# Performance work log

Measured on AMD Instinct MI355X. Metric: run time of the kernel, lower is better.

The kernel has to match this reference:

```python
import jax, jax.numpy as jnp
import numpy as np

C = 1.0          # curvature parameter (constraint <x,x>_L = -1/C)
EPS = 1e-7
N_NODES = 50000
D = 128
N_EDGES = 800000


def _l_inner(u, v):
    # Lorentz (Minkowski) inner product: -u0*v0 + <u_s, v_s>
    return -u[..., 0] * v[..., 0] + jnp.sum(u[..., 1:] * v[..., 1:], axis=-1)


def _proj(x, c=C):
    # recompute time coordinate so x lies on the hyperboloid
    sp = x[:, 1:]
    x0 = jnp.sqrt(1.0 / c + jnp.sum(sp * sp, axis=-1, keepdims=True))
    return jnp.concatenate([x0, sp], axis=-1)


def _logmap0(x, c=C):
    sqc = jnp.sqrt(c)
    x0, sp = x[:, :1], x[:, 1:]
    y = jnp.clip(sqc * x0, 1.0 + EPS, None)
    d = jnp.arccosh(y) / sqc                                   # geodesic distance to origin
    sn = jnp.clip(jnp.linalg.norm(sp, axis=-1, keepdims=True), EPS, None)
    return jnp.concatenate([jnp.zeros_like(x0), d * sp / sn], axis=-1)


def _expmap0(u, c=C):
    sqc = jnp.sqrt(c)
    sp = u[:, 1:]
    un = jnp.clip(jnp.linalg.norm(sp, axis=-1, keepdims=True), EPS, None)
    th = sqc * un
    x0 = jnp.cosh(th) / sqc
    return jnp.concatenate([x0, jnp.sinh(th) * sp / th], axis=-1)


def setup_inputs() -> dict:
    key = jax.random.key(0)
    k1, k2, k3 = jax.random.split(key, 3)
    x_raw = jax.random.normal(k1, (N_NODES, D), dtype=jnp.float32) * 0.5
    x = _proj(x_raw)  # valid points on the Lorentz manifold
    # xavier-uniform-like scale for (127,127) weight
    lim = float(np.sqrt(6.0 / (2 * (D - 1))))
    weight = jax.random.uniform(k2, (D - 1, D - 1), dtype=jnp.float32, minval=-lim, maxval=lim)
    bias = jnp.zeros((D - 1,), dtype=jnp.float32)
    edge_index = jax.random.randint(k3, (2, N_EDGES), 0, N_NODES, dtype=jnp.int64)
    return {"x": x, "weight": weight, "bias": bias, "edge_index": edge_index}


def reference(x, weight, bias, edge_index):
    c = C
    # ---- HyperbolicLinear (lorentz): log0 -> spatial matmul + bias -> exp0 -> proj
    v = _logmap0(x, c)                         # [N, D], time comp = 0
    out_space = v[:, 1:] @ weight.T + bias     # [N, D-1]
    out = jnp.concatenate([v[:, :1], out_space], axis=-1)
    h = _proj(_expmap0(out, c), c)             # [N, D] on manifold
    # ---- HyperbolicDistAtt: gather -> lorentz distance -> exp(-d)
    row, col = edge_index[0], edge_index[1]
    xi = h[row]                                # [E, D]
    xj = h[col]                                # [E, D]
    inner = _l_inner(xi, xj)                   # [E]
    dist = jnp.arccosh(jnp.clip(-c * inner, 1.0 + EPS, None)) / jnp.sqrt(c)
    att = jnp.exp(-dist)                       # [E]
    # ---- Lorentz centroid: weighted sum then Minkowski-norm normalization
    num = jax.ops.segment_sum(att[:, None] * xj, row, num_segments=h.shape[0])  # [N, D]
    denom = jnp.sqrt(c) * jnp.sqrt(jnp.clip(-_l_inner(num, num), EPS, None))    # [N]
    return num / denom[:, None]
```

## Files before the change

### kernel.cpp

```cpp
#include <hip/hip_runtime.h>
#include <math.h>

#define EPS 1e-7f
#define CAP 64
#define REC_INTS   34
#define REC_USH    68
#define LIST_OFF    4

typedef __attribute__((ext_vector_type(8))) short short8;
typedef __attribute__((ext_vector_type(4))) float floatx4;
typedef _Float16 half2v __attribute__((ext_vector_type(2)));

__device__ inline short f2bf(float f) {
    union { float f; unsigned u; } v; v.f = f;
    unsigned r = v.u + 0x7FFF + ((v.u >> 16) & 1);
    return (short)(r >> 16);
}
__device__ inline ushort f2h(float f) {
    union { _Float16 h; ushort u; } v; v.h = (_Float16)f; return v.u;
}
__device__ inline half2v u2h2(unsigned u) {
    union { unsigned x; half2v h; } v; v.x = u; return v.h;
}
__device__ inline float dot2acc(unsigned a, unsigned b, float c) {
#if __has_builtin(__builtin_amdgcn_fdot2)
    return __builtin_amdgcn_fdot2(u2h2(a), u2h2(b), c, false);
#else
    half2v ha = u2h2(a), hb = u2h2(b);
    return c + (float)ha[0] * (float)hb[0] + (float)ha[1] * (float)hb[1];
#endif
}

__device__ inline float fast_sqrt(float x) { return __builtin_amdgcn_sqrtf(x); }
__device__ inline float fast_rcp(float x)  { return __builtin_amdgcn_rcpf(x); }
__device__ inline float fast_rsq(float x)  { return __builtin_amdgcn_rsqf(x); }

__global__ __launch_bounds__(256) void prep_w(
    const float* __restrict__ weight, short* __restrict__ wfg,
    int* __restrict__ rec, int N)
{
    int idx = blockIdx.x * 256 + threadIdx.x;
    if (idx < 128 * 128) {
        int j = idx >> 7, k = idx & 127;
        float w = (j < 127 && k >= 1) ? weight[j * 127 + (k - 1)] : 0.0f;
        int tt = j >> 4, cc = j & 15, ss = k >> 5, qq = (k >> 3) & 3, ee = k & 7;
        wfg[(((tt * 4 + ss) * 64) + qq * 16 + cc) * 8 + ee] = f2bf(w);
    }
    if (rec) {
        for (int r = idx; r < N; r += gridDim.x * 256) rec[(size_t)r * REC_INTS] = 0;
    }
}

__global__ __launch_bounds__(256) void transform16(
    const float* __restrict__ x, const short* __restrict__ wfg,
    const float* __restrict__ bias, ushort* __restrict__ h16, int N)
{
    __shared__ __align__(16) short Vf[4 * 4 * 64 * 8];

    const int t = threadIdx.x;
    const int lane = t & 63;
    const int wv = t >> 6;
    const int c = lane & 15;
    const int q = lane >> 4;

    float bvals[8];
    #pragma unroll
    for (int tt = 0; tt < 8; ++tt) {
        int j = tt * 16 + c;
        bvals[tt] = (j < 127) ? bias[j] : 0.0f;
    }

    const short8* wfp = (const short8*)wfg;
    const short8* vfp = (const short8*)Vf + wv * 256;
    short8* vw = (short8*)Vf;

    const int nchunks = (N + 63) >> 6;
    for (int chunk = blockIdx.x; chunk < nchunks; chunk += gridDim.x) {
        const int base = chunk * 64;

        {
            int nl = t >> 2;
            int qt = t & 3;
            int n = base + nl;
            const float4* xr = (const float4*)(x + (size_t)n * 128 + qt * 32);
            float4 xv[8];
            if (n < N) {
                #pragma unroll
                for (int g = 0; g < 8; ++g) xv[g] = xr[g];
            } else {
                #pragma unroll
                for (int g = 0; g < 8; ++g) xv[g] = make_float4(0, 0, 0, 0);
            }
            float ss = 0.0f;
            #pragma unroll
            for (int g = 0; g < 8; ++g)
                ss += xv[g].x * xv[g].x + xv[g].y * xv[g].y +
                      xv[g].z * xv[g].z + xv[g].w * xv[g].w;
            float x0 = xv[0].x;
            if (qt == 0) ss -= x0 * x0;
            ss += __shfl_xor(ss, 1, 64);
            ss += __shfl_xor(ss, 2, 64);
            x0 = __shfl(x0, lane & ~3, 64);
            float sn = fmaxf(fast_sqrt(ss), EPS);
            float xc = fmaxf(x0, 1.0f + EPS);
            float dd = __logf(xc + fast_sqrt(xc * xc - 1.0f));
            float coef = dd * fast_rcp(sn);
            int wreg = nl >> 4, cn = nl & 15;
            #pragma unroll
            for (int g = 0; g < 4; ++g) {
                float4 a = xv[2 * g], b = xv[2 * g + 1];
                short8 pk;
                pk[0] = f2bf(coef * a.x); pk[1] = f2bf(coef * a.y);
                pk[2] = f2bf(coef * a.z); pk[3] = f2bf(coef * a.w);
                pk[4] = f2bf(coef * b.x); pk[5] = f2bf(coef * b.y);
                pk[6] = f2bf(coef * b.z); pk[7] = f2bf(coef * b.w);
                vw[wreg * 256 + qt * 64 + g * 16 + cn] = pk;
            }
        }

        floatx4 acc[8];
        #pragma unroll
        for (int tt = 0; tt < 8; ++tt) acc[tt] = (floatx4){0, 0, 0, 0};
        #pragma unroll
        for (int s = 0; s < 4; ++s) {
            short8 af = vfp[s * 64 + lane];
            #pragma unroll
            for (int tt = 0; tt < 8; ++tt) {
                short8 bf = wfp[(tt * 4 + s) * 64 + lane];
                acc[tt] = __builtin_amdgcn_mfma_f32_16x16x32_bf16(af, bf, acc[tt], 0, 0, 0);
            }
        }

        float rs[4] = {0, 0, 0, 0};
        #pragma unroll
        for (int tt = 0; tt < 8; ++tt) {
            #pragma unroll
            for (int r = 0; r < 4; ++r) {
                float v = acc[tt][r] + bvals[tt];
                acc[tt][r] = v;
                rs[r] += v * v;
            }
        }
        #pragma unroll
        for (int r = 0; r < 4; ++r) {
            rs[r] += __shfl_xor(rs[r], 1, 64);
            rs[r] += __shfl_xor(rs[r], 2, 64);
            rs[r] += __shfl_xor(rs[r], 4, 64);
            rs[r] += __shfl_xor(rs[r], 8, 64);
        }
        int nodebase = base + wv * 16 + q * 4;
        #pragma unroll
        for (int r = 0; r < 4; ++r) {
            int n = nodebase + r;
            if (n < N) {
                float th = fmaxf(fast_sqrt(rs[r]), EPS);
                float ex = __expf(th);
                float sc_big = (ex - fast_rcp(ex)) * 0.5f * fast_rcp(th);
                float sc_small = 1.0f + th * th * (1.0f / 6.0f);
                float scale = (th < 1e-3f) ? sc_small : sc_big;
                ushort* hr = h16 + (size_t)n * 128;
                #pragma unroll
                for (int tt = 0; tt < 8; ++tt) {
                    int p = tt * 16 + c;
                    if (p < 127) hr[p] = f2h(scale * acc[tt][r]);
                    else hr[127] = f2h(fast_sqrt(1.0f + scale * scale * rs[r]));
                }
            }
        }
    }
}

__global__ __launch_bounds__(256) void scatter_cap(
    const int* __restrict__ rows, const int* __restrict__ cols,
    int* __restrict__ rec, int E)
{
    int base = blockIdx.x * 1024 + (int)threadIdx.x;
    int r[4], c[4], p[4];
    bool val[4];
    #pragma unroll
    for (int e = 0; e < 4; ++e) {
        int i = base + 256 * e;
        val[e] = i < E;
        r[e] = 0; c[e] = 0;
        if (val[e]) {
            r[e] = __builtin_nontemporal_load(rows + i);
            c[e] = __builtin_nontemporal_load(cols + i);
        }
    }
    #pragma unroll
    for (int e = 0; e < 4; ++e)
        if (val[e]) p[e] = atomicAdd(rec + (size_t)r[e] * REC_INTS, 1);
    #pragma unroll
    for (int e = 0; e < 4; ++e)
        if (val[e] && p[e] < CAP)
            ((ushort*)rec)[(size_t)r[e] * REC_USH + LIST_OFF + p[e]] = (ushort)c[e];
}

__global__ __launch_bounds__(256) void agg_cap16(
    const ushort* __restrict__ h16, const int* __restrict__ rec,
    float* __restrict__ out, int N)
{
    int wid = (int)((blockIdx.x * 256u + threadIdx.x) >> 6);
    int nw = (int)(gridDim.x * 4u);
    int lane = threadIdx.x & 63;
    int q = lane >> 4;
    int i = lane & 15;

    for (int n = wid; n < N; n += nw) {
        const ushort* lst = (const ushort*)rec + (size_t)n * REC_USH + LIST_OFF;
        int ec = (int)lst[lane];
        int deg = rec[(size_t)n * REC_INTS];
        if (deg > CAP) deg = CAP;

        uint4 wn = *(const uint4*)(h16 + (size_t)n * 128 + 8 * i);
        if (i == 15) wn.w ^= 0x80000000u;
        float acc[8] = {0, 0, 0, 0, 0, 0, 0, 0};

        for (int kb = 0; kb < deg; kb += 16) {
            int k0 = kb + q;
            bool v[4];
            int cc[4];
            uint4 w[4];
            #pragma unroll
            for (int e = 0; e < 4; ++e) {
                int kk = k0 + 4 * e;
                v[e] = kk < deg;
                cc[e] = __shfl(ec, kk, 64);
                w[e] = make_uint4(0, 0, 0, 0);
                if (v[e])
                    w[e] = *(const uint4*)(h16 + (size_t)cc[e] * 128 + 8 * i);
            }
            float s[4];
            #pragma unroll
            for (int e = 0; e < 4; ++e) {
                float d = dot2acc(wn.x, w[e].x, 0.0f);
                d = dot2acc(wn.y, w[e].y, d);
                d = dot2acc(wn.z, w[e].z, d);
                s[e] = dot2acc(wn.w, w[e].w, d);
            }
            #pragma unroll
            for (int o = 1; o <= 8; o <<= 1) {
                #pragma unroll
                for (int e = 0; e < 4; ++e) s[e] += __shfl_xor(s[e], o, 64);
            }
            float att[4];
            #pragma unroll
            for (int e = 0; e < 4; ++e) {
                float z = fmaxf(-s[e], 1.0f + EPS);
                float a = fast_rcp(z + fast_sqrt(z * z - 1.0f));
                if (cc[e] == n) a = 1.0f;
                att[e] = v[e] ? a : 0.0f;
            }
            #pragma unroll
            for (int e = 0; e < 4; ++e) {
                union { uint4 u; _Float16 h[8]; } wu; wu.u = w[e];
                #pragma unroll
                for (int m = 0; m < 8; ++m)
                    acc[m] += att[e] * (float)wu.h[m];
            }
        }

        #pragma unroll
        for (int k = 0; k < 8; ++k) {
            acc[k] += __shfl_xor(acc[k], 16, 64);
            acc[k] += __shfl_xor(acc[k], 32, 64);
        }

        float part = 0.0f;
        #pragma unroll
        for (int k = 0; k < 8; ++k) part -= acc[k] * acc[k];
        if (i == 15) part += 2.0f * acc[7] * acc[7];
        #pragma unroll
        for (int o = 1; o <= 8; o <<= 1) part += __shfl_xor(part, o, 64);
        float inv = fast_rsq(fmaxf(part, EPS));

        if (q == 0) {
            float* orow = out + (size_t)n * 128;
            #pragma unroll
            for (int m = 0; m < 8; ++m) {
                int p = 8 * i + m;
                float vv = acc[m] * inv;
                if (p == 127) orow[0] = vv;
                else          orow[1 + p] = vv;
            }
        }
    }
}

__global__ __launch_bounds__(256) void transform_mfma(
    const float* __restrict__ x, const short* __restrict__ wfg,
    const float* __restrict__ bias, float* __restrict__ h, int N)
{
    __shared__ __align__(16) short Vf[4 * 4 * 64 * 8];

    const int t = threadIdx.x;
    const int lane = t & 63;
    const int wv = t >> 6;
    const int c = lane & 15;
    const int q = lane >> 4;

    float bvals[8];
    #pragma unroll
    for (int tt = 0; tt < 8; ++tt) {
        int j = tt * 16 + c;
        bvals[tt] = (j < 127) ? bias[j] : 0.0f;
    }

    const short8* wfp = (const short8*)wfg;
    const short8* vfp = (const short8*)Vf + wv * 256;
    short8* vw = (short8*)Vf;

    const int nchunks = (N + 63) >> 6;
    for (int chunk = blockIdx.x; chunk < nchunks; chunk += gridDim.x) {
        const int base = chunk * 64;
        {
            int nl = t >> 2;
            int qt = t & 3;
            int n = base + nl;
            const float4* xr = (const float4*)(x + (size_t)n * 128 + qt * 32);
            float4 xv[8];
            if (n < N) {
                #pragma unroll
                for (int g = 0; g < 8; ++g) xv[g] = xr[g];
            } else {
                #pragma unroll
                for (int g = 0; g < 8; ++g) xv[g] = make_float4(0, 0, 0, 0);
            }
            float ss = 0.0f;
            #pragma unroll
            for (int g = 0; g < 8; ++g)
                ss += xv[g].x * xv[g].x + xv[g].y * xv[g].y +
                      xv[g].z * xv[g].z + xv[g].w * xv[g].w;
            float x0 = xv[0].x;
            if (qt == 0) ss -= x0 * x0;
            ss += __shfl_xor(ss, 1, 64);
            ss += __shfl_xor(ss, 2, 64);
            x0 = __shfl(x0, lane & ~3, 64);
            float sn = fmaxf(fast_sqrt(ss), EPS);
            float xc = fmaxf(x0, 1.0f + EPS);
            float dd = __logf(xc + fast_sqrt(xc * xc - 1.0f));
            float coef = dd * fast_rcp(sn);
            int wreg = nl >> 4, cn = nl & 15;
            #pragma unroll
            for (int g = 0; g < 4; ++g) {
                float4 a = xv[2 * g], b = xv[2 * g + 1];
                short8 pk;
                pk[0] = f2bf(coef * a.x); pk[1] = f2bf(coef * a.y);
                pk[2] = f2bf(coef * a.z); pk[3] = f2bf(coef * a.w);
                pk[4] = f2bf(coef * b.x); pk[5] = f2bf(coef * b.y);
                pk[6] = f2bf(coef * b.z); pk[7] = f2bf(coef * b.w);
                vw[wreg * 256 + qt * 64 + g * 16 + cn] = pk;
            }
        }

        floatx4 acc[8];
        #pragma unroll
        for (int tt = 0; tt < 8; ++tt) acc[tt] = (floatx4){0, 0, 0, 0};
        #pragma unroll
        for (int s = 0; s < 4; ++s) {
            short8 af = vfp[s * 64 + lane];
            #pragma unroll
            for (int tt = 0; tt < 8; ++tt) {
                short8 bf = wfp[(tt * 4 + s) * 64 + lane];
                acc[tt] = __builtin_amdgcn_mfma_f32_16x16x32_bf16(af, bf, acc[tt], 0, 0, 0);
            }
        }

        float rs[4] = {0, 0, 0, 0};
        #pragma unroll
        for (int tt = 0; tt < 8; ++tt) {
            #pragma unroll
            for (int r = 0; r < 4; ++r) {
                float v = acc[tt][r] + bvals[tt];
                acc[tt][r] = v;
                rs[r] += v * v;
            }
        }
        #pragma unroll
        for (int r = 0; r < 4; ++r) {
            rs[r] += __shfl_xor(rs[r], 1, 64);
            rs[r] += __shfl_xor(rs[r], 2, 64);
            rs[r] += __shfl_xor(rs[r], 4, 64);
            rs[r] += __shfl_xor(rs[r], 8, 64);
        }
        int nodebase = base + wv * 16 + q * 4;
        #pragma unroll
        for (int r = 0; r < 4; ++r) {
            int n = nodebase + r;
            if (n < N) {
                float th = fmaxf(fast_sqrt(rs[r]), EPS);
                float ex = __expf(th);
                float sc_big = (ex - fast_rcp(ex)) * 0.5f * fast_rcp(th);
                float sc_small = 1.0f + th * th * (1.0f / 6.0f);
                float scale = (th < 1e-3f) ? sc_small : sc_big;
                float* hr = h + (size_t)n * 128;
                #pragma unroll
                for (int tt = 0; tt < 8; ++tt) {
                    int j = tt * 16 + c;
                    if (j < 127) hr[1 + j] = scale * acc[tt][r];
                    else         hr[0] = fast_sqrt(1.0f + scale * scale * rs[r]);
                }
            }
        }
    }
}

__global__ __launch_bounds__(256) void hist_kernel(
    const int* __restrict__ rows, int* __restrict__ deg, int E)
{
    int i = blockIdx.x * 256 + threadIdx.x;
    if (i < E) atomicAdd(&deg[rows[i]], 1);
}

__global__ __launch_bounds__(1024) void scan1(
    const int* __restrict__ deg, int* __restrict__ off,
    int* __restrict__ bsum, int N)
{
    __shared__ int wsum[16];
    __shared__ int wexcl[16];
    int i = blockIdx.x * 1024 + threadIdx.x;
    int lane = threadIdx.x & 63, wid = threadIdx.x >> 6;
    int v = (i < N) ? deg[i] : 0;
    int incl = v;
    #pragma unroll
    for (int o = 1; o < 64; o <<= 1) {
        int u = __shfl_up(incl, o, 64);
        if (lane >= o) incl += u;
    }
    if (lane == 63) wsum[wid] = incl;
    __syncthreads();
    if (wid == 0 && lane < 16) {
        int s = wsum[lane];
        int si = s;
        #pragma unroll
        for (int o = 1; o < 16; o <<= 1) {
            int u = __shfl_up(si, o, 64);
            if (lane >= o) si += u;
        }
        wexcl[lane] = si - s;
        if (lane == 15) bsum[blockIdx.x] = si;
    }
    __syncthreads();
    if (i < N) off[i] = wexcl[wid] + incl - v;
}

__global__ __launch_bounds__(64) void scan2(int* __restrict__ bsum, int nb)
{
    int lane = threadIdx.x & 63;
    int v = (lane < nb) ? bsum[lane] : 0;
    int si = v;
    #pragma unroll
    for (int o = 1; o < 64; o <<= 1) {
        int u = __shfl_up(si, o, 64);
        if (lane >= o) si += u;
    }
    if (lane < nb) bsum[lane] = si - v;
}

__global__ __launch_bounds__(1024) void scan3(
    int* __restrict__ off, int* __restrict__ pos,
    const int* __restrict__ bsum, int N, int E)
{
    int i = blockIdx.x * 1024 + threadIdx.x;
    if (i < N) {
        int v = off[i] + bsum[blockIdx.x];
        off[i] = v;
        pos[i] = v;
    }
    if (i == 0) off[N] = E;
}

__global__ __launch_bounds__(256) void scatter_kernel(
    const int* __restrict__ rows, const int* __restrict__ cols,
    int* __restrict__ pos, int* __restrict__ ecol, int E)
{
    int i = blockIdx.x * 256 + threadIdx.x;
    if (i < E) {
        int p = atomicAdd(&pos[rows[i]], 1);
        ecol[p] = cols[i];
    }
}

__global__ __launch_bounds__(256) void agg_kernel(
    const float* __restrict__ h, const int* __restrict__ off,
    const int* __restrict__ ecol, float* __restrict__ out, int N)
{
    int wid = (int)((blockIdx.x * 256u + threadIdx.x) >> 6);
    int nw = (int)(gridDim.x * 4u);
    int lane = threadIdx.x & 63;
    int q = lane >> 4;
    int i = lane & 15;

    for (int n = wid; n < N; n += nw) {
        const float4* hn = (const float4*)(h + (size_t)n * 128) + 2 * i;
        float4 xa = hn[0], xb = hn[1];
        float xa0 = (i == 0) ? -xa.x : xa.x;
        float acc[8] = {0, 0, 0, 0, 0, 0, 0, 0};
        int e0 = off[n], e1 = off[n + 1];

        int e = e0 + q;
        for (; e + 4 < e1; e += 8) {
            int c0 = ecol[e];
            int c1 = ecol[e + 4];
            const float4* p0 = (const float4*)(h + (size_t)c0 * 128) + 2 * i;
            const float4* p1 = (const float4*)(h + (size_t)c1 * 128) + 2 * i;
            float4 a0 = p0[0], b0 = p0[1];
            float4 a1 = p1[0], b1 = p1[1];
            float s0 = xa0 * a0.x + xa.y * a0.y + xa.z * a0.z + xa.w * a0.w
                     + xb.x * b0.x + xb.y * b0.y + xb.z * b0.z + xb.w * b0.w;
            float s1 = xa0 * a1.x + xa.y * a1.y + xa.z * a1.z + xa.w * a1.w
                     + xb.x * b1.x + xb.y * b1.y + xb.z * b1.z + xb.w * b1.w;
            #pragma unroll
            for (int o = 1; o <= 8; o <<= 1) {
                s0 += __shfl_xor(s0, o, 64);
                s1 += __shfl_xor(s1, o, 64);
            }
            float z0 = fmaxf(-s0, 1.0f + EPS);
            float z1 = fmaxf(-s1, 1.0f + EPS);
            float att0 = fast_rcp(z0 + fast_sqrt(z0 * z0 - 1.0f));
            float att1 = fast_rcp(z1 + fast_sqrt(z1 * z1 - 1.0f));
            acc[0] += att0 * a0.x + att1 * a1.x;
            acc[1] += att0 * a0.y + att1 * a1.y;
            acc[2] += att0 * a0.z + att1 * a1.z;
            acc[3] += att0 * a0.w + att1 * a1.w;
            acc[4] += att0 * b0.x + att1 * b1.x;
            acc[5] += att0 * b0.y + att1 * b1.y;
            acc[6] += att0 * b0.z + att1 * b1.z;
            acc[7] += att0 * b0.w + att1 * b1.w;
        }
        if (e < e1) {
            int c0 = ecol[e];
            const float4* p0 = (const float4*)(h + (size_t)c0 * 128) + 2 * i;
            float4 a0 = p0[0], b0 = p0[1];
            float s0 = xa0 * a0.x + xa.y * a0.y + xa.z * a0.z + xa.w * a0.w
                     + xb.x * b0.x + xb.y * b0.y + xb.z * b0.z + xb.w * b0.w;
            #pragma unroll
            for (int o = 1; o <= 8; o <<= 1) s0 += __shfl_xor(s0, o, 64);
            float z0 = fmaxf(-s0, 1.0f + EPS);
            float att0 = fast_rcp(z0 + fast_sqrt(z0 * z0 - 1.0f));
            acc[0] += att0 * a0.x;
            acc[1] += att0 * a0.y;
            acc[2] += att0 * a0.z;
            acc[3] += att0 * a0.w;
            acc[4] += att0 * b0.x;
            acc[5] += att0 * b0.y;
            acc[6] += att0 * b0.z;
            acc[7] += att0 * b0.w;
        }

        #pragma unroll
        for (int k = 0; k < 8; ++k) {
            acc[k] += __shfl_xor(acc[k], 16, 64);
            acc[k] += __shfl_xor(acc[k], 32, 64);
        }

        float part = 0.0f;
        #pragma unroll
        for (int k = 0; k < 8; ++k) part -= acc[k] * acc[k];
        if (i == 0) part += 2.0f * acc[0] * acc[0];
        #pragma unroll
        for (int o = 1; o <= 8; o <<= 1) part += __shfl_xor(part, o, 64);
        float inv = fast_rsq(fmaxf(part, EPS));

        if (q == 0) {
            float4* op = (float4*)(out + (size_t)n * 128) + 2 * i;
            op[0] = make_float4(acc[0] * inv, acc[1] * inv, acc[2] * inv, acc[3] * inv);
            op[1] = make_float4(acc[4] * inv, acc[5] * inv, acc[6] * inv, acc[7] * inv);
        }
    }
}

__global__ __launch_bounds__(256) void edge_kernel(
    const float* __restrict__ h, const int* __restrict__ rows,
    const int* __restrict__ cols, float* __restrict__ num, int E)
{
    int wid = (int)((blockIdx.x * 256u + threadIdx.x) >> 6);
    if (wid >= E) return;
    int lane = threadIdx.x & 63;
    int r = rows[wid];
    int c = cols[wid];
    const float2* h2 = (const float2*)h;
    float2 xi = h2[(size_t)r * 64 + lane];
    float2 xj = h2[(size_t)c * 64 + lane];
    float p = (lane == 0 ? -xi.x * xj.x : xi.x * xj.x) + xi.y * xj.y;
    #pragma unroll
    for (int off = 32; off >= 1; off >>= 1) p += __shfl_xor(p, off, 64);
    float z = fmaxf(-p, 1.0f + EPS);
    float att = fast_rcp(z + fast_sqrt(z * z - 1.0f));
    float* dst = num + (size_t)r * 128 + 2 * lane;
    atomicAdd(dst, att * xj.x);
    atomicAdd(dst + 1, att * xj.y);
}

__global__ __launch_bounds__(256) void norm_kernel(float* __restrict__ num, int N)
{
    int wid = (int)((blockIdx.x * 256u + threadIdx.x) >> 6);
    int nw = (int)((gridDim.x * 256u) >> 6);
    int lane = threadIdx.x & 63;
    for (int n = wid; n < N; n += nw) {
        float2* p2 = (float2*)(num + (size_t)n * 128);
        float2 v = p2[lane];
        float q = (lane == 0) ? (v.x * v.x - v.y * v.y) : (-v.x * v.x - v.y * v.y);
        #pragma unroll
        for (int o = 32; o >= 1; o >>= 1) q += __shfl_xor(q, o, 64);
        float inv = fast_rsq(fmaxf(q, EPS));
        p2[lane] = make_float2(v.x * inv, v.y * inv);
    }
}

extern "C" void kernel_launch(void* const* d_in, const int* in_sizes, int n_in,
                              void* d_out, int out_size, void* d_ws, size_t ws_size,
                              hipStream_t stream)
{
    const float* x      = (const float*)d_in[0];
    const float* weight = (const float*)d_in[1];
    const float* bias   = (const float*)d_in[2];
    const int*   edge   = (const int*)d_in[3];

    const int N = in_sizes[0] / 128;
    const int E = in_sizes[3] / 2;
    const int* rows = edge;
    const int* cols = edge + E;

    const int nchunks = (N + 63) >> 6;

    {
        char* base = (char*)d_ws;
        ushort* h16 = (ushort*)base;                 base += (size_t)N * 128 * 2;
        short* wfg  = (short*)base;                  base += (size_t)128 * 128 * 2;
        int* rec    = (int*)base;
        size_t need_cap = (size_t)((char*)rec - (char*)d_ws) + (size_t)N * REC_INTS * 4;

        if (ws_size >= need_cap && N <= 65535) {
            prep_w<<<256, 256, 0, stream>>>(weight, wfg, rec, N);
            transform16<<<nchunks, 256, 0, stream>>>(x, wfg, bias, h16, N);
            scatter_cap<<<(E + 1023) / 1024, 256, 0, stream>>>(rows, cols, rec, E);
            agg_cap16<<<(N + 3) / 4, 256, 0, stream>>>(h16, rec, (float*)d_out, N);
            return;
        }
    }

    char* base = (char*)d_ws;
    float* h   = (float*)base;                       base += (size_t)N * 128 * 4;
    short* wfg = (short*)base;                       base += (size_t)128 * 128 * 2;
    char* rest = base;
    size_t head = (size_t)(rest - (char*)d_ws);

    int* deg  = (int*)rest;
    int* off  = deg + N;
    int* pos  = off + (N + 1);
    int* bsum = pos + N;
    int* ecol = bsum + 64;
    size_t need_csr = head + ((size_t)N * 3 + 65 + E) * 4;

    if (ws_size >= need_csr) {
        prep_w<<<256, 256, 0, stream>>>(weight, wfg, deg, N);
        transform_mfma<<<nchunks, 256, 0, stream>>>(x, wfg, bias, h, N);
        const int nsb = (N + 1023) / 1024;
        hist_kernel<<<(E + 255) / 256, 256, 0, stream>>>(rows, deg, E);
        scan1<<<nsb, 1024, 0, stream>>>(deg, off, bsum, N);
        scan2<<<1, 64, 0, stream>>>(bsum, nsb);
        scan3<<<nsb, 1024, 0, stream>>>(off, pos, bsum, N, E);
        scatter_kernel<<<(E + 255) / 256, 256, 0, stream>>>(rows, cols, pos, ecol, E);
        agg_kernel<<<(N + 3) / 4, 256, 0, stream>>>(h, off, ecol, (float*)d_out, N);
    } else {
        prep_w<<<256, 256, 0, stream>>>(weight, wfg, (int*)nullptr, 0);
        transform_mfma<<<nchunks, 256, 0, stream>>>(x, wfg, bias, h, N);
        hipMemsetAsync(d_out, 0, (size_t)out_size * sizeof(float), stream);
        edge_kernel<<<(E + 3) / 4, 256, 0, stream>>>(h, rows, cols, (float*)d_out, E);
        norm_kernel<<<2048, 256, 0, stream>>>((float*)d_out, N);
    }
}
```

Before: 169.9 us.

## Fuse transform and edge scatter into one interleaved kernel launch

Merges the node transform kernel and the capped edge scatter kernel into a single launch, where even blocks run transform chunks and odd blocks run scatter batches. The aim is to overlap compute-heavy matmul work with atomic-heavy scatter work and to remove one kernel launch boundary. In exchange, scatter blocks also reserve the transform's shared memory, which can lower occupancy, and the interleaving depends on the two block counts being similar.

Measured after the change: 182.1 us. 7.2% more time.

```diff
diff --git a/kernel.cpp b/kernel.cpp
--- a/kernel.cpp
+++ b/kernel.cpp
@@ -51,9 +51,10 @@
     }
 }
 
-__global__ __launch_bounds__(256) void transform16(
+__device__ __forceinline__ void transform16_body(
     const float* __restrict__ x, const short* __restrict__ wfg,
-    const float* __restrict__ bias, ushort* __restrict__ h16, int N)
+    const float* __restrict__ bias, ushort* __restrict__ h16, int N,
+    int chunk0, int cstride)
 {
     __shared__ __align__(16) short Vf[4 * 4 * 64 * 8];
 
@@ -75,7 +76,7 @@
     short8* vw = (short8*)Vf;
 
     const int nchunks = (N + 63) >> 6;
-    for (int chunk = blockIdx.x; chunk < nchunks; chunk += gridDim.x) {
+    for (int chunk = chunk0; chunk < nchunks; chunk += cstride) {
         const int base = chunk * 64;
 
         {
@@ -170,11 +171,18 @@
     }
 }
 
-__global__ __launch_bounds__(256) void scatter_cap(
+__global__ __launch_bounds__(256) void transform16(
+    const float* __restrict__ x, const short* __restrict__ wfg,
+    const float* __restrict__ bias, ushort* __restrict__ h16, int N)
+{
+    transform16_body(x, wfg, bias, h16, N, blockIdx.x, gridDim.x);
+}
+
+__device__ __forceinline__ void scatter4_body(
     const int* __restrict__ rows, const int* __restrict__ cols,
-    int* __restrict__ rec, int E)
-{
-    int base = blockIdx.x * 1024 + (int)threadIdx.x;
+    int* __restrict__ rec, int E, int sb)
+{
+    int base = sb * 1024 + (int)threadIdx.x;
     int r[4], c[4], p[4];
     bool val[4];
     #pragma unroll
@@ -194,6 +202,28 @@
     for (int e = 0; e < 4; ++e)
         if (val[e] && p[e] < CAP)
             ((ushort*)rec)[(size_t)r[e] * REC_USH + LIST_OFF + p[e]] = (ushort)c[e];
+}
+
+__global__ __launch_bounds__(256) void scatter_cap(
+    const int* __restrict__ rows, const int* __restrict__ cols,
+    int* __restrict__ rec, int E)
+{
+    scatter4_body(rows, cols, rec, E, (int)blockIdx.x);
+}
+
+__global__ __launch_bounds__(256) void fused_ts(
+    const float* __restrict__ x, const short* __restrict__ wfg,
+    const float* __restrict__ bias, ushort* __restrict__ h16, int N,
+    const int* __restrict__ rows, const int* __restrict__ cols,
+    int* __restrict__ rec, int E, int T, int S)
+{
+    int bid = (int)blockIdx.x;
+    int m = bid >> 1;
+    if ((bid & 1) == 0) {
+        if (m < T) transform16_body(x, wfg, bias, h16, N, m, (int)gridDim.x);
+    } else {
+        if (m < S) scatter4_body(rows, cols, rec, E, m);
+    }
 }
 
 __global__ __launch_bounds__(256) void agg_cap16(
@@ -632,9 +662,12 @@
         size_t need_cap = (size_t)((char*)rec - (char*)d_ws) + (size_t)N * REC_INTS * 4;
 
         if (ws_size >= need_cap && N <= 65535) {
+            const int T = nchunks;
+            const int S = (E + 1023) / 1024;
+            const int G = 2 * (T > S ? T : S);
             prep_w<<<256, 256, 0, stream>>>(weight, wfg, rec, N);
-            transform16<<<nchunks, 256, 0, stream>>>(x, wfg, bias, h16, N);
-            scatter_cap<<<(E + 1023) / 1024, 256, 0, stream>>>(rows, cols, rec, E);
+            fused_ts<<<G, 256, 0, stream>>>(x, wfg, bias, h16, N,
+                                            rows, cols, rec, E, T, S);
             agg_cap16<<<(N + 3) / 4, 256, 0, stream>>>(h16, rec, (float*)d_out, N);
             return;
         }
```
